# Kernel tuning notes

Measured on AMD Instinct MI355X. Metric: run time of the kernel, lower is better.

The kernel has to match this reference:

```python
import jax, jax.numpy as jnp
from jax import lax
import numpy as np

SEQ, B, DI, DL, V = 512, 64, 512, 1024, 50257

def setup_inputs() -> dict:
    key = jax.random.key(0)
    ks = jax.random.split(key, 6)
    X = jax.random.randint(ks[0], (SEQ, B), 0, V, dtype=jnp.int64)
    h = jax.random.normal(ks[1], (B, DL), dtype=jnp.float32)
    emb = jax.random.normal(ks[2], (V, DI), dtype=jnp.float32) * 0.02
    W_z = jax.random.normal(ks[3], (DL + DI, DL), dtype=jnp.float32) * 0.02
    W_r = jax.random.normal(ks[4], (DL + DI, DL), dtype=jnp.float32) * 0.02
    W_h = jax.random.normal(ks[5], (DL + DI, DL), dtype=jnp.float32) * 0.02
    return {"X": X, "h": h, "emb": emb, "W_z": W_z, "W_r": W_r, "W_h": W_h}

def reference(X, h, emb, W_z, W_r, W_h):
    # X: [S, B] int token ids; h: [B, DL]; returns H: [S, B, DL]
    def step(h_prev, x_t):
        x_emb = emb[x_t]                                   # [B, DI]
        mc = jnp.concatenate([h_prev, x_emb], axis=1)      # [B, DL+DI]
        z = jax.nn.sigmoid(mc @ W_z)                       # update gate
        r = jax.nn.sigmoid(mc @ W_r)                       # reset gate
        cand = jnp.tanh(jnp.concatenate([r * h_prev, x_emb], axis=1) @ W_h)
        h_new = (1.0 - z) * h_prev + z * cand
        return h_new, h_new
    _, H = lax.scan(step, h, X)
    return H
```

## Files before the change

kernel.cpp:

```cpp
#include <hip/hip_runtime.h>

typedef _Float16 f16;
typedef _Float16 f16x4 __attribute__((ext_vector_type(4)));
typedef _Float16 f16x8 __attribute__((ext_vector_type(8)));
typedef float    f32x4 __attribute__((ext_vector_type(4)));

#define MFMA16(a, b, c) __builtin_amdgcn_mfma_f32_16x16x32_f16(a, b, c, 0, 0, 0)

static constexpr int kS  = 512;
static constexpr int kB  = 64;
static constexpr int kDI = 512;
static constexpr int kDL = 1024;
static constexpr int kV  = 50257;

union U128 { unsigned long long q[2]; f16x8 v; };

static __device__ __forceinline__ void store_llc_f16(f16* p, f16 v) {
  unsigned v32 = (unsigned)__builtin_bit_cast(unsigned short, v);
  asm volatile("global_store_short %0, %1, off sc0 sc1" :: "v"(p), "v"(v32) : "memory");
}

static __device__ __forceinline__ void wait_phase(const unsigned* flags, unsigned goal, int lane) {
  for (;;) {
    unsigned f = __hip_atomic_load(flags + lane, __ATOMIC_RELAXED, __HIP_MEMORY_SCOPE_AGENT);
    if (__all((int)(f >= goal))) return;
    __builtin_amdgcn_s_sleep(1);
  }
}

static __device__ __forceinline__ void drain_and_signal(unsigned* flags, int wg, int tid, unsigned seq) {
  asm volatile("s_waitcnt vmcnt(0)" ::: "memory");
  __syncthreads();
  if (tid == 0)
    asm volatile("global_store_dword %0, %1, off sc0 sc1" :: "v"(flags + wg), "v"(seq) : "memory");
}

__global__ void k_emb_convert(const float* __restrict__ src, f16* __restrict__ dst, int n4) {
  int i = blockIdx.x * 256 + threadIdx.x;
  if (i >= n4) return;
  float4 v = ((const float4*)src)[i];
  f16x4 o = {(f16)v.x, (f16)v.y, (f16)v.z, (f16)v.w};
  ((f16x4*)dst)[i] = o;
}

__global__ void k_pack_bot(const float* __restrict__ Wz, const float* __restrict__ Wr,
                           const float* __restrict__ Wh, f16* __restrict__ Bpk) {
  int tid = blockIdx.x * 256 + threadIdx.x;
  int lane = tid & 63, kstep = (tid >> 6) & 15, ntile = tid >> 10;
  int n = ntile * 16 + (lane & 15);
  const float* W = (n < 1024) ? Wz : (n < 2048 ? Wr : Wh);
  int ncol = n & 1023;
  int kbase = kstep * 32 + (lane >> 4) * 8;
  f16x8 v;
#pragma unroll
  for (int j = 0; j < 8; ++j) v[j] = (f16)W[(size_t)(1024 + kbase + j) * 1024 + ncol];
  ((f16x8*)Bpk)[tid] = v;
}

__global__ void k_pack_top(const float* __restrict__ Wz, const float* __restrict__ Wr,
                           const float* __restrict__ Wh, f16* __restrict__ Tpk) {
  int tid = blockIdx.x * 256 + threadIdx.x;
  int lane = tid & 63, kstep = (tid >> 6) & 31, wg = (tid >> 11) & 63, m = tid >> 17;
  const float* W = (m == 0) ? Wz : (m == 1 ? Wr : Wh);
  int col = wg * 16 + (lane & 15);
  int kbase = kstep * 32 + (lane >> 4) * 8;
  f16x8 v;
#pragma unroll
  for (int j = 0; j < 8; ++j) v[j] = (f16)W[(size_t)(kbase + j) * 1024 + col];
  ((f16x8*)Tpk)[tid] = v;
}

__global__ void k_h_convert(const float* __restrict__ h0, f16* __restrict__ hfrag) {
  int i = blockIdx.x * 256 + threadIdx.x;
  int slot = i & 3, ln = (i >> 2) & 63, wsel = (i >> 8) & 1, frag = i >> 9;
  int ks = frag & 31, mt = frag >> 5;
  int b = mt * 16 + (ln & 15);
  int k = ks * 32 + (ln >> 4) * 8 + wsel * 4 + slot;
  hfrag[i] = (f16)h0[(size_t)b * kDL + k];
}

__global__ __launch_bounds__(256, 2)
void k_xproj(const int* __restrict__ X, const f16* __restrict__ emb16,
             const f16* __restrict__ Bpk, f16* Xzr, f16* __restrict__ Xh) {
  const int bm = blockIdx.x / 24, bn = blockIdx.x % 24;
  const int tid = threadIdx.x;
  const int w = tid >> 6, lane = tid & 63, l15 = lane & 15, quad = lane >> 4;

  __shared__ int tok[128];
  __shared__ f16x8 Asm[8 * 2 * 64];
  __shared__ f16x8 Bsm[8 * 2 * 64];

  if (tid < 128) tok[tid] = X[bm * 128 + tid];
  __syncthreads();

  f32x4 zero4 = {0.f, 0.f, 0.f, 0.f};
  f32x4 acc[4][4];
#pragma unroll
  for (int i = 0; i < 4; ++i)
#pragma unroll
    for (int j = 0; j < 4; ++j) acc[i][j] = zero4;

  const int mtb = (w & 1) * 4, ntb = (w >> 1) * 4;

  for (int ki = 0; ki < 8; ++ki) {
#pragma unroll
    for (int c = 0; c < 4; ++c) {
      int cid = c * 256 + tid;
      int r = cid >> 3, kc = cid & 7;
      Asm[((r >> 4) * 2 + (kc >> 2)) * 64 + (kc & 3) * 16 + (r & 15)] =
          *(const f16x8*)(emb16 + (size_t)tok[r] * kDI + ki * 64 + kc * 8);
    }
#pragma unroll
    for (int c = 0; c < 4; ++c) {
      int cid = c * 256 + tid;
      int nt = cid >> 7, ks = (cid >> 6) & 1, ln = cid & 63;
      Bsm[cid] = ((const f16x8*)Bpk)[((size_t)(bn * 8 + nt) * 16 + (ki * 2 + ks)) * 64 + ln];
    }
    __syncthreads();
#pragma unroll
    for (int ks = 0; ks < 2; ++ks) {
      f16x8 a[4], b[4];
#pragma unroll
      for (int i = 0; i < 4; ++i) a[i] = Asm[((mtb + i) * 2 + ks) * 64 + lane];
#pragma unroll
      for (int j = 0; j < 4; ++j) b[j] = Bsm[((ntb + j) * 2 + ks) * 64 + lane];
#pragma unroll
      for (int i = 0; i < 4; ++i)
#pragma unroll
        for (int j = 0; j < 4; ++j) acc[i][j] = MFMA16(a[i], b[j], acc[i][j]);
    }
    __syncthreads();
  }

  const int rowb = bm * 128 + (w & 1) * 64;
  const int colb = bn * 128 + (w >> 1) * 64;
#pragma unroll
  for (int i = 0; i < 4; ++i)
#pragma unroll
    for (int j = 0; j < 4; ++j)
#pragma unroll
      for (int reg = 0; reg < 4; ++reg) {
        int row = rowb + i * 16 + quad * 4 + reg;
        int col = colb + j * 16 + l15;
        f16 v = (f16)acc[i][j][reg];
        if (col < 2048) Xzr[(size_t)row * 2048 + col] = v;
        else            Xh[(size_t)row * 1024 + (col - 2048)] = v;
      }
}

__global__ __launch_bounds__(256, 1)
void k_gru(const float* __restrict__ h0, const f16* __restrict__ Tpk,
           const f16* Xzr , const f16* __restrict__ Xh,
           f16* hfrag, f16* rhfrag, unsigned* flags, float* H) {
  const int wg = blockIdx.x;
  const int tid = threadIdx.x;
  const int w = tid >> 6, lane = tid & 63, l15 = lane & 15, quad = lane >> 4;
  const int colbase = wg * 16;

  __shared__ f32x4 red[4][4][2][64];

  f32x4 zero4 = {0.f, 0.f, 0.f, 0.f};

  const f16x8* T = (const f16x8*)Tpk;
  f16x8 wz[8], wr[8], wh[8];
#pragma unroll
  for (int s = 0; s < 8; ++s) {
    int ks = w * 8 + s;
    wz[s] = T[((0 * 64 + wg) * 32 + ks) * 64 + lane];
    wr[s] = T[((1 * 64 + wg) * 32 + ks) * 64 + lane];
    wh[s] = T[((2 * 64 + wg) * 32 + ks) * 64 + lane];
  }

  float hreg[4];
#pragma unroll
  for (int r4 = 0; r4 < 4; ++r4) {
    int b = w * 16 + quad * 4 + r4;
    hreg[r4] = h0[(size_t)b * kDL + colbase + l15];
  }

  const int lane_dst0 = ((wg & 1) * 2 + (l15 >> 3)) * 16 + quad * 4;
  const int scat = ((w * 32 + (wg >> 1)) * 128 + ((l15 >> 2) & 1) * 64 + lane_dst0) * 4 + (l15 & 3);
  f16* const rh_p = rhfrag + scat;
  f16* const h_p  = hfrag  + scat;

  const unsigned long long* hq = (const unsigned long long*)hfrag;
  const unsigned long long* rq = (const unsigned long long*)rhfrag;

  unsigned seq = 0;

#pragma unroll 1
  for (int t = 0; t < kS; ++t) {
    float xz[4], xr[4];
#pragma unroll
    for (int r4 = 0; r4 < 4; ++r4) {
      int b = w * 16 + quad * 4 + r4;
      size_t xi = ((size_t)t * kB + b) * 2048 + colbase + l15;
      xz[r4] = (float)Xzr[xi];
      xr[r4] = (float)Xzr[xi + 1024];
    }

    wait_phase(flags, seq, lane);

    f16x8 af[8][4];
#pragma unroll
    for (int mt = 0; mt < 4; ++mt) {
      const unsigned long long* pm = hq + (size_t)(mt * 32 + w * 8) * 128 + lane;
#pragma unroll
      for (int s = 0; s < 8; ++s) {
        U128 u;
        u.q[0] = __hip_atomic_load(pm + s * 128,      __ATOMIC_RELAXED, __HIP_MEMORY_SCOPE_AGENT);
        u.q[1] = __hip_atomic_load(pm + s * 128 + 64, __ATOMIC_RELAXED, __HIP_MEMORY_SCOPE_AGENT);
        af[s][mt] = u.v;
      }
    }

    f32x4 az[4], ar[4];
#pragma unroll
    for (int mt = 0; mt < 4; ++mt) { az[mt] = zero4; ar[mt] = zero4; }
#pragma unroll
    for (int s = 0; s < 8; ++s)
#pragma unroll
      for (int mt = 0; mt < 4; ++mt) {
        az[mt] = MFMA16(af[s][mt], wz[s], az[mt]);
        ar[mt] = MFMA16(af[s][mt], wr[s], ar[mt]);
      }

#pragma unroll
    for (int mt = 0; mt < 4; ++mt) { red[w][mt][0][lane] = az[mt]; red[w][mt][1][lane] = ar[mt]; }
    __syncthreads();
    f32x4 zs = red[0][w][0][lane] + red[1][w][0][lane] + red[2][w][0][lane] + red[3][w][0][lane];
    f32x4 rs = red[0][w][1][lane] + red[1][w][1][lane] + red[2][w][1][lane] + red[3][w][1][lane];

    float zreg[4];
#pragma unroll
    for (int r4 = 0; r4 < 4; ++r4) {
      float zin = zs[r4] + xz[r4];
      float rin = rs[r4] + xr[r4];
      float z = 1.f / (1.f + __expf(-zin));
      float r = 1.f / (1.f + __expf(-rin));
      zreg[r4] = z;
      store_llc_f16(rh_p + r4 * 4, (f16)(r * hreg[r4]));
    }
    drain_and_signal(flags, wg, tid, ++seq);

    float xh[4];
#pragma unroll
    for (int r4 = 0; r4 < 4; ++r4) {
      int b = w * 16 + quad * 4 + r4;
      xh[r4] = (float)Xh[((size_t)t * kB + b) * kDL + colbase + l15];
    }

    wait_phase(flags, seq, lane);

    f16x8 bf[8][4];
#pragma unroll
    for (int mt = 0; mt < 4; ++mt) {
      const unsigned long long* pm = rq + (size_t)(mt * 32 + w * 8) * 128 + lane;
#pragma unroll
      for (int s = 0; s < 8; ++s) {
        U128 u;
        u.q[0] = __hip_atomic_load(pm + s * 128,      __ATOMIC_RELAXED, __HIP_MEMORY_SCOPE_AGENT);
        u.q[1] = __hip_atomic_load(pm + s * 128 + 64, __ATOMIC_RELAXED, __HIP_MEMORY_SCOPE_AGENT);
        bf[s][mt] = u.v;
      }
    }

    f32x4 ac[4];
#pragma unroll
    for (int mt = 0; mt < 4; ++mt) ac[mt] = zero4;
#pragma unroll
    for (int s = 0; s < 8; ++s)
#pragma unroll
      for (int mt = 0; mt < 4; ++mt)
        ac[mt] = MFMA16(bf[s][mt], wh[s], ac[mt]);

#pragma unroll
    for (int mt = 0; mt < 4; ++mt) red[w][mt][0][lane] = ac[mt];
    __syncthreads();
    f32x4 cs = red[0][w][0][lane] + red[1][w][0][lane] + red[2][w][0][lane] + red[3][w][0][lane];

#pragma unroll
    for (int r4 = 0; r4 < 4; ++r4) {
      int b = w * 16 + quad * 4 + r4;
      float cin = cs[r4] + xh[r4];
      float cand = 1.f - 2.f / (__expf(2.f * cin) + 1.f);
      float hn = hreg[r4] + zreg[r4] * (cand - hreg[r4]);
      hreg[r4] = hn;
      H[((size_t)t * kB + b) * kDL + colbase + l15] = hn;
      store_llc_f16(h_p + r4 * 4, (f16)hn);
    }
    drain_and_signal(flags, wg, tid, ++seq);
  }
}

extern "C" void kernel_launch(void* const* d_in, const int* in_sizes, int n_in,
                              void* d_out, int out_size, void* d_ws, size_t ws_size,
                              hipStream_t stream) {
  const int*   X   = (const int*)d_in[0];
  const float* h0  = (const float*)d_in[1];
  const float* emb = (const float*)d_in[2];
  const float* Wz  = (const float*)d_in[3];
  const float* Wr  = (const float*)d_in[4];
  const float* Wh  = (const float*)d_in[5];
  float* H = (float*)d_out;

  char* ws = (char*)d_ws;
  size_t o = 0;
  f16* emb16 = (f16*)(ws + o); o += (size_t)kV * kDI * 2;
  f16* Bpk   = (f16*)(ws + o); o += (size_t)3072 * 512 * 2;
  f16* Tpk   = (f16*)(ws + o); o += (size_t)3 * 1024 * 1024 * 2;
  f16* hfrag = (f16*)(ws + o); o += (size_t)kB * kDL * 2;
  f16* rhfrag= (f16*)(ws + o); o += (size_t)kB * kDL * 2;
  unsigned* flags = (unsigned*)(ws + o); o += 256;
  f16* Xh    = (f16*)(ws + o); o += (size_t)kS * kB * kDL * 2;
  f16* Xzr = (f16*)d_out;

  hipMemsetAsync(flags, 0, 256, stream);

  int n4 = kV * kDI / 4;
  k_emb_convert<<<(n4 + 255) / 256, 256, 0, stream>>>(emb, emb16, n4);
  k_pack_bot<<<196608 / 256, 256, 0, stream>>>(Wz, Wr, Wh, Bpk);
  k_pack_top<<<393216 / 256, 256, 0, stream>>>(Wz, Wr, Wh, Tpk);
  k_h_convert<<<65536 / 256, 256, 0, stream>>>(h0, hfrag);
  k_xproj<<<256 * 24, 256, 0, stream>>>(X, emb16, Bpk, Xzr, Xh);
  k_gru<<<64, 256, 0, stream>>>(h0, Tpk, Xzr, Xh, hfrag, rhfrag, flags, H);
}
```

Measured before the change: 5.988 ms.

## Split GRU recurrence into independent batch groups with per-group sync and full-K waves

The recurrent kernel splits the batch into 4 independent groups of 16 rows. Each group's 16 blocks synchronise only among themselves through 16 flags, instead of all 64 blocks waiting on 64 flags. Each wave now owns one 16-column tile across the full K range, with z/r weights held in registers and Wh staged in LDS, which removes the cross-wave LDS reduction and its __syncthreads per phase. The h/r*h fragment layout and the h_convert kernel change to match. The cost is much higher register pressure (64 f16x8 weight fragments plus 32 activation fragments per wave) and a serial 32-step MFMA chain per wave.

```diff
diff --git a/kernel.cpp b/kernel.cpp
--- a/kernel.cpp
+++ b/kernel.cpp
@@ -13,6 +13,10 @@
 static constexpr int kDL = 1024;
 static constexpr int kV  = 50257;
 
+static constexpr int NGRP = 4;
+static constexpr int GSZ  = 16;
+static constexpr int NBLK = NGRP * GSZ;
+
 union U128 { unsigned long long q[2]; f16x8 v; };
 
 static __device__ __forceinline__ void store_llc_f16(f16* p, f16 v) {
@@ -20,19 +24,20 @@
   asm volatile("global_store_short %0, %1, off sc0 sc1" :: "v"(p), "v"(v32) : "memory");
 }
 
-static __device__ __forceinline__ void wait_phase(const unsigned* flags, unsigned goal, int lane) {
+static __device__ __forceinline__ void wait_phase(const unsigned* flg, unsigned goal, int lane) {
+  const unsigned* p = flg + (lane & 15);
   for (;;) {
-    unsigned f = __hip_atomic_load(flags + lane, __ATOMIC_RELAXED, __HIP_MEMORY_SCOPE_AGENT);
+    unsigned f = __hip_atomic_load(p, __ATOMIC_RELAXED, __HIP_MEMORY_SCOPE_AGENT);
     if (__all((int)(f >= goal))) return;
     __builtin_amdgcn_s_sleep(1);
   }
 }
 
-static __device__ __forceinline__ void drain_and_signal(unsigned* flags, int wg, int tid, unsigned seq) {
+static __device__ __forceinline__ void drain_signal(unsigned* myflag, int tid, unsigned seq) {
   asm volatile("s_waitcnt vmcnt(0)" ::: "memory");
   __syncthreads();
   if (tid == 0)
-    asm volatile("global_store_dword %0, %1, off sc0 sc1" :: "v"(flags + wg), "v"(seq) : "memory");
+    asm volatile("global_store_dword %0, %1, off sc0 sc1" :: "v"(myflag), "v"(seq) : "memory");
 }
 
 __global__ void k_emb_convert(const float* __restrict__ src, f16* __restrict__ dst, int n4) {
@@ -72,11 +77,13 @@
 
 __global__ void k_h_convert(const float* __restrict__ h0, f16* __restrict__ hfrag) {
   int i = blockIdx.x * 256 + threadIdx.x;
-  int slot = i & 3, ln = (i >> 2) & 63, wsel = (i >> 8) & 1, frag = i >> 9;
-  int ks = frag & 31, mt = frag >> 5;
-  int b = mt * 16 + (ln & 15);
-  int k = ks * 32 + (ln >> 4) * 8 + wsel * 4 + slot;
-  hfrag[i] = (f16)h0[(size_t)b * kDL + k];
+  int lane = i & 63, plane = (i >> 6) & 1, ks = (i >> 7) & 31, g = i >> 12;
+  int row = g * 16 + (lane & 15);
+  int k = ks * 32 + (lane >> 4) * 8 + plane * 4;
+  f16x4 v;
+#pragma unroll
+  for (int j = 0; j < 4; ++j) v[j] = (f16)h0[(size_t)row * kDL + k + j];
+  ((f16x4*)hfrag)[i] = v;
 }
 
 __global__ __launch_bounds__(256, 2)
@@ -151,145 +158,124 @@
 __global__ __launch_bounds__(256, 1)
 void k_gru(const float* __restrict__ h0, const f16* __restrict__ Tpk,
            const f16* Xzr , const f16* __restrict__ Xh,
-           f16* hfrag, f16* rhfrag, unsigned* flags, float* H) {
-  const int wg = blockIdx.x;
+           f16* hfrag, f16* rhfrag, unsigned* sync, float* H) {
+  __shared__ f16x8 ldsWh[4 * 32 * 64];
+
+  const int g = blockIdx.x >> 4, blk = blockIdx.x & 15;
   const int tid = threadIdx.x;
   const int w = tid >> 6, lane = tid & 63, l15 = lane & 15, quad = lane >> 4;
-  const int colbase = wg * 16;
-
-  __shared__ f32x4 red[4][4][2][64];
-
-  f32x4 zero4 = {0.f, 0.f, 0.f, 0.f};
 
   const f16x8* T = (const f16x8*)Tpk;
-  f16x8 wz[8], wr[8], wh[8];
-#pragma unroll
-  for (int s = 0; s < 8; ++s) {
-    int ks = w * 8 + s;
-    wz[s] = T[((0 * 64 + wg) * 32 + ks) * 64 + lane];
-    wr[s] = T[((1 * 64 + wg) * 32 + ks) * 64 + lane];
-    wh[s] = T[((2 * 64 + wg) * 32 + ks) * 64 + lane];
-  }
-
-  float hreg[4];
-#pragma unroll
-  for (int r4 = 0; r4 < 4; ++r4) {
-    int b = w * 16 + quad * 4 + r4;
-    hreg[r4] = h0[(size_t)b * kDL + colbase + l15];
-  }
-
-  const int lane_dst0 = ((wg & 1) * 2 + (l15 >> 3)) * 16 + quad * 4;
-  const int scat = ((w * 32 + (wg >> 1)) * 128 + ((l15 >> 2) & 1) * 64 + lane_dst0) * 4 + (l15 & 3);
+  const int tile = blk * 4 + w;
+  const int c    = tile * 16 + l15;
+
+  f16x8 wz[32], wr[32];
+#pragma unroll
+  for (int s = 0; s < 32; ++s) {
+    wz[s] = T[((size_t)(0 * 64 + tile) * 32 + s) * 64 + lane];
+    wr[s] = T[((size_t)(1 * 64 + tile) * 32 + s) * 64 + lane];
+  }
+#pragma unroll 4
+  for (int it = 0; it < 32; ++it) {
+    int idx = it * 256 + tid;
+    ldsWh[idx] = T[(size_t)(128 + blk * 4 + (idx >> 11)) * 2048 + (idx & 2047)];
+  }
+  __syncthreads();
+
+  const int rowb = g * 16;
+
+  float hreg[4], zreg[4];
+#pragma unroll
+  for (int r4 = 0; r4 < 4; ++r4)
+    hreg[r4] = h0[(size_t)(rowb + quad * 4 + r4) * kDL + c];
+
+  const int ks_s  = tile >> 1;
+  const int qp    = (w & 1) * 2 + (l15 >> 3);
+  const int plane = (l15 >> 2) & 1;
+  const size_t scat =
+      (((size_t)g * 4096) + ((size_t)ks_s * 2 + plane) * 64 + qp * 16 + quad * 4) * 4 + (l15 & 3);
   f16* const rh_p = rhfrag + scat;
-  f16* const h_p  = hfrag  + scat;
-
-  const unsigned long long* hq = (const unsigned long long*)hfrag;
-  const unsigned long long* rq = (const unsigned long long*)rhfrag;
-
+  f16* const h_p  = hfrag + scat;
+
+  const unsigned long long* hq = (const unsigned long long*)hfrag + (size_t)g * 4096 + lane;
+  const unsigned long long* rq = (const unsigned long long*)rhfrag + (size_t)g * 4096 + lane;
+
+  unsigned* flg = sync + g * 32;
   unsigned seq = 0;
 
 #pragma unroll 1
   for (int t = 0; t < kS; ++t) {
-    float xz[4], xr[4];
+    float xz[4], xr[4], xh[4];
 #pragma unroll
     for (int r4 = 0; r4 < 4; ++r4) {
-      int b = w * 16 + quad * 4 + r4;
-      size_t xi = ((size_t)t * kB + b) * 2048 + colbase + l15;
-      xz[r4] = (float)Xzr[xi];
-      xr[r4] = (float)Xzr[xi + 1024];
-    }
-
-    wait_phase(flags, seq, lane);
-
-    f16x8 af[8][4];
-#pragma unroll
-    for (int mt = 0; mt < 4; ++mt) {
-      const unsigned long long* pm = hq + (size_t)(mt * 32 + w * 8) * 128 + lane;
-#pragma unroll
-      for (int s = 0; s < 8; ++s) {
-        U128 u;
-        u.q[0] = __hip_atomic_load(pm + s * 128,      __ATOMIC_RELAXED, __HIP_MEMORY_SCOPE_AGENT);
-        u.q[1] = __hip_atomic_load(pm + s * 128 + 64, __ATOMIC_RELAXED, __HIP_MEMORY_SCOPE_AGENT);
-        af[s][mt] = u.v;
-      }
-    }
-
-    f32x4 az[4], ar[4];
-#pragma unroll
-    for (int mt = 0; mt < 4; ++mt) { az[mt] = zero4; ar[mt] = zero4; }
-#pragma unroll
-    for (int s = 0; s < 8; ++s)
-#pragma unroll
-      for (int mt = 0; mt < 4; ++mt) {
-        az[mt] = MFMA16(af[s][mt], wz[s], az[mt]);
-        ar[mt] = MFMA16(af[s][mt], wr[s], ar[mt]);
-      }
-
-#pragma unroll
-    for (int mt = 0; mt < 4; ++mt) { red[w][mt][0][lane] = az[mt]; red[w][mt][1][lane] = ar[mt]; }
-    __syncthreads();
-    f32x4 zs = red[0][w][0][lane] + red[1][w][0][lane] + red[2][w][0][lane] + red[3][w][0][lane];
-    f32x4 rs = red[0][w][1][lane] + red[1][w][1][lane] + red[2][w][1][lane] + red[3][w][1][lane];
-
-    float zreg[4];
+      size_t row = (size_t)t * kB + rowb + quad * 4 + r4;
+      xz[r4] = (float)Xzr[row * 2048 + c];
+      xr[r4] = (float)Xzr[row * 2048 + 1024 + c];
+      xh[r4] = (float)Xh[row * 1024 + c];
+    }
+
+    wait_phase(flg, seq, lane);
+
+    f16x8 af[32];
+#pragma unroll
+    for (int s = 0; s < 32; ++s) {
+      U128 u;
+      u.q[0] = __hip_atomic_load(hq + s * 128,      __ATOMIC_RELAXED, __HIP_MEMORY_SCOPE_AGENT);
+      u.q[1] = __hip_atomic_load(hq + s * 128 + 64, __ATOMIC_RELAXED, __HIP_MEMORY_SCOPE_AGENT);
+      af[s] = u.v;
+    }
+
+    f32x4 az0 = {0.f,0.f,0.f,0.f}, az1 = {0.f,0.f,0.f,0.f};
+    f32x4 ar0 = {0.f,0.f,0.f,0.f}, ar1 = {0.f,0.f,0.f,0.f};
+#pragma unroll
+    for (int s = 0; s < 32; s += 2) {
+      az0 = MFMA16(af[s],     wz[s],     az0);
+      ar0 = MFMA16(af[s],     wr[s],     ar0);
+      az1 = MFMA16(af[s + 1], wz[s + 1], az1);
+      ar1 = MFMA16(af[s + 1], wr[s + 1], ar1);
+    }
+    f32x4 zsum = az0 + az1, rsum = ar0 + ar1;
+
 #pragma unroll
     for (int r4 = 0; r4 < 4; ++r4) {
-      float zin = zs[r4] + xz[r4];
-      float rin = rs[r4] + xr[r4];
+      float zin = zsum[r4] + xz[r4];
+      float rin = rsum[r4] + xr[r4];
       float z = 1.f / (1.f + __expf(-zin));
       float r = 1.f / (1.f + __expf(-rin));
       zreg[r4] = z;
       store_llc_f16(rh_p + r4 * 4, (f16)(r * hreg[r4]));
     }
-    drain_and_signal(flags, wg, tid, ++seq);
-
-    float xh[4];
+    drain_signal(flg + blk, tid, ++seq);
+
+    wait_phase(flg, seq, lane);
+
+    f16x8 bf[32];
+#pragma unroll
+    for (int s = 0; s < 32; ++s) {
+      U128 u;
+      u.q[0] = __hip_atomic_load(rq + s * 128,      __ATOMIC_RELAXED, __HIP_MEMORY_SCOPE_AGENT);
+      u.q[1] = __hip_atomic_load(rq + s * 128 + 64, __ATOMIC_RELAXED, __HIP_MEMORY_SCOPE_AGENT);
+      bf[s] = u.v;
+    }
+
+    f32x4 ac0 = {0.f,0.f,0.f,0.f}, ac1 = {0.f,0.f,0.f,0.f};
+#pragma unroll
+    for (int s = 0; s < 32; s += 2) {
+      ac0 = MFMA16(bf[s],     ldsWh[(w * 32 + s) * 64 + lane],     ac0);
+      ac1 = MFMA16(bf[s + 1], ldsWh[(w * 32 + s + 1) * 64 + lane], ac1);
+    }
+    f32x4 csum = ac0 + ac1;
+
 #pragma unroll
     for (int r4 = 0; r4 < 4; ++r4) {
-      int b = w * 16 + quad * 4 + r4;
-      xh[r4] = (float)Xh[((size_t)t * kB + b) * kDL + colbase + l15];
-    }
-
-    wait_phase(flags, seq, lane);
-
-    f16x8 bf[8][4];
-#pragma unroll
-    for (int mt = 0; mt < 4; ++mt) {
-      const unsigned long long* pm = rq + (size_t)(mt * 32 + w * 8) * 128 + lane;
-#pragma unroll
-      for (int s = 0; s < 8; ++s) {
-        U128 u;
-        u.q[0] = __hip_atomic_load(pm + s * 128,      __ATOMIC_RELAXED, __HIP_MEMORY_SCOPE_AGENT);
-        u.q[1] = __hip_atomic_load(pm + s * 128 + 64, __ATOMIC_RELAXED, __HIP_MEMORY_SCOPE_AGENT);
-        bf[s][mt] = u.v;
-      }
-    }
-
-    f32x4 ac[4];
-#pragma unroll
-    for (int mt = 0; mt < 4; ++mt) ac[mt] = zero4;
-#pragma unroll
-    for (int s = 0; s < 8; ++s)
-#pragma unroll
-      for (int mt = 0; mt < 4; ++mt)
-        ac[mt] = MFMA16(bf[s][mt], wh[s], ac[mt]);
-
-#pragma unroll
-    for (int mt = 0; mt < 4; ++mt) red[w][mt][0][lane] = ac[mt];
-    __syncthreads();
-    f32x4 cs = red[0][w][0][lane] + red[1][w][0][lane] + red[2][w][0][lane] + red[3][w][0][lane];
-
-#pragma unroll
-    for (int r4 = 0; r4 < 4; ++r4) {
-      int b = w * 16 + quad * 4 + r4;
-      float cin = cs[r4] + xh[r4];
+      float cin = csum[r4] + xh[r4];
       float cand = 1.f - 2.f / (__expf(2.f * cin) + 1.f);
       float hn = hreg[r4] + zreg[r4] * (cand - hreg[r4]);
       hreg[r4] = hn;
-      H[((size_t)t * kB + b) * kDL + colbase + l15] = hn;
+      H[((size_t)t * kB + rowb + quad * 4 + r4) * kDL + c] = hn;
       store_llc_f16(h_p + r4 * 4, (f16)hn);
     }
-    drain_and_signal(flags, wg, tid, ++seq);
+    drain_signal(flg + blk, tid, ++seq);
   }
 }
 
@@ -309,19 +295,19 @@
   f16* emb16 = (f16*)(ws + o); o += (size_t)kV * kDI * 2;
   f16* Bpk   = (f16*)(ws + o); o += (size_t)3072 * 512 * 2;
   f16* Tpk   = (f16*)(ws + o); o += (size_t)3 * 1024 * 1024 * 2;
-  f16* hfrag = (f16*)(ws + o); o += (size_t)kB * kDL * 2;
-  f16* rhfrag= (f16*)(ws + o); o += (size_t)kB * kDL * 2;
-  unsigned* flags = (unsigned*)(ws + o); o += 256;
+  f16* hfrag = (f16*)(ws + o); o += (size_t)NGRP * 4096 * 8;
+  f16* rhfrag= (f16*)(ws + o); o += (size_t)NGRP * 4096 * 8;
+  unsigned* sync = (unsigned*)(ws + o); o += 1024;
   f16* Xh    = (f16*)(ws + o); o += (size_t)kS * kB * kDL * 2;
   f16* Xzr = (f16*)d_out;
 
-  hipMemsetAsync(flags, 0, 256, stream);
+  hipMemsetAsync(sync, 0, 1024, stream);
 
   int n4 = kV * kDI / 4;
   k_emb_convert<<<(n4 + 255) / 256, 256, 0, stream>>>(emb, emb16, n4);
   k_pack_bot<<<196608 / 256, 256, 0, stream>>>(Wz, Wr, Wh, Bpk);
   k_pack_top<<<393216 / 256, 256, 0, stream>>>(Wz, Wr, Wh, Tpk);
-  k_h_convert<<<65536 / 256, 256, 0, stream>>>(h0, hfrag);
+  k_h_convert<<<64, 256, 0, stream>>>(h0, hfrag);
   k_xproj<<<256 * 24, 256, 0, stream>>>(X, emb16, Bpk, Xzr, Xh);
-  k_gru<<<64, 256, 0, stream>>>(h0, Tpk, Xzr, Xh, hfrag, rhfrag, flags, H);
-}
+  k_gru<<<NBLK, 256, 0, stream>>>(h0, Tpk, Xzr, Xh, hfrag, rhfrag, sync, H);
+}
```

Result: slower. 8.234 ms (+37.5%).
